# Kernel optimization log

Hardware: AMD Instinct MI355X
Metric: run time of the kernel (lower is better)

The kernel has to match this reference:

```python
import jax, jax.numpy as jnp
import numpy as np

B, T, D, H = 512, 1024, 64, 64     # batch, time, input_size, hidden_size
R = 4                              # number of reward heads
MH = 32                            # MLP hidden size


def setup_inputs() -> dict:
    key = jax.random.key(0)
    ks = jax.random.split(key, 16)
    s = lambda k, shape, scale=1.0: jax.random.normal(k, shape, dtype=jnp.float32) * scale
    inp = {
        "x": s(ks[0], (B, T, D)),
        # learned initial states (nn.Parameter randn(1,1,H) -> store as (H,))
        "h_init": s(ks[1], (H,)),
        "c_init": s(ks[2], (H,)),
        # LSTM params, PyTorch layout: W_ih (4H, D), W_hh (4H, H), gate order i,f,g,o
        "W_ih": s(ks[3], (4 * H, D), 1.0 / np.sqrt(H)),
        "W_hh": s(ks[4], (4 * H, H), 1.0 / np.sqrt(H)),
        "b_ih": s(ks[5], (4 * H,), 1.0 / np.sqrt(H)),
        "b_hh": s(ks[6], (4 * H,), 1.0 / np.sqrt(H)),
        # R stacked MLP heads: Linear(H,MH) -> ReLU -> Linear(MH,MH) -> ReLU -> Linear(MH,1)
        "W1": s(ks[7], (R, MH, H), 1.0 / np.sqrt(H)),
        "b1": s(ks[8], (R, MH), 1.0 / np.sqrt(H)),
        "W2": s(ks[9], (R, MH, MH), 1.0 / np.sqrt(MH)),
        "b2": s(ks[10], (R, MH), 1.0 / np.sqrt(MH)),
        "W3": s(ks[11], (R, 1, MH), 1.0 / np.sqrt(MH)),
        "b3": s(ks[12], (R, 1), 1.0 / np.sqrt(MH)),
    }
    return inp


def _lstm(x, h0, c0, W_ih, W_hh, b_ih, b_hh):
    # x: (B, T, D). Returns y: (B, T, H).
    Hh = h0.shape[-1]
    b = b_ih + b_hh                      # (4H,)
    # precompute input projections for all steps: (T, B, 4H)
    xg = jnp.einsum('btd,gd->tbg', x, W_ih) + b

    def step(carry, xg_t):
        h, c = carry                     # (B, H) each
        gates = xg_t + h @ W_hh.T        # (B, 4H)
        i, f, g, o = jnp.split(gates, 4, axis=-1)
        c = jax.nn.sigmoid(f) * c + jax.nn.sigmoid(i) * jnp.tanh(g)
        h = jax.nn.sigmoid(o) * jnp.tanh(c)
        return (h, c), h

    Bb = x.shape[0]
    h0b = jnp.broadcast_to(h0, (Bb, Hh))
    c0b = jnp.broadcast_to(c0, (Bb, Hh))
    _, ys = jax.lax.scan(step, (h0b, c0b), xg)   # ys: (T, B, H)
    return jnp.transpose(ys, (1, 0, 2))


def _heads(y, W1, b1, W2, b2, W3, b3):
    # y: (B, T, H) -> (R, B, T); all R heads computed in one batched einsum chain
    h1 = jax.nn.relu(jnp.einsum('bth,rmh->rbtm', y, W1) + b1[:, None, None, :])
    h2 = jax.nn.relu(jnp.einsum('rbtm,rnm->rbtn', h1, W2) + b2[:, None, None, :])
    out = jnp.einsum('rbtn,ron->rbto', h2, W3) + b3[:, None, None, :]
    return out[..., 0]                   # squeeze last dim -> (R, B, T)


def reference(x, h_init, c_init, W_ih, W_hh, b_ih, b_hh, W1, b1, W2, b2, W3, b3):
    y = _lstm(x, h_init, c_init, W_ih, W_hh, b_ih, b_hh)
    outs = _heads(y, W1, b1, W2, b2, W3, b3)   # (R, B, T); row r == rewards[r] head
    return (y, outs)
```

## Files before the change

kernel.cpp:

```cpp
#include <hip/hip_runtime.h>

#define BB 512
#define TT 1024
#define DD 64
#define HH 64
#define G4 256
#define RR 4
#define MHH 32
#define BT (BB * TT)
#define Y_SIZE (BB * TT * HH)

typedef _Float16 half8 __attribute__((ext_vector_type(8)));
typedef _Float16 half4 __attribute__((ext_vector_type(4)));
typedef float f32x4 __attribute__((ext_vector_type(4)));

#define MFMA16(a, b, c) __builtin_amdgcn_mfma_f32_16x16x32_f16((a), (b), (c), 0, 0, 0)

__device__ __forceinline__ void wg_barrier_lds() {
    asm volatile("s_waitcnt lgkmcnt(0)" ::: "memory");
    __builtin_amdgcn_s_barrier();
    asm volatile("" ::: "memory");
}

__device__ __forceinline__ float sigm(float x) {
    return __builtin_amdgcn_rcpf(1.0f + __expf(-x));
}
__device__ __forceinline__ float tanh_(float x) {
    return 1.0f - 2.0f * __builtin_amdgcn_rcpf(1.0f + __expf(2.0f * x));
}

__device__ __forceinline__ half8 cvt8(f32x4 a, f32x4 b) {
    half8 h;
    h[0] = (_Float16)a[0]; h[1] = (_Float16)a[1];
    h[2] = (_Float16)a[2]; h[3] = (_Float16)a[3];
    h[4] = (_Float16)b[0]; h[5] = (_Float16)b[1];
    h[6] = (_Float16)b[2]; h[7] = (_Float16)b[3];
    return h;
}

__global__ __launch_bounds__(256) void lstm_kernel(
    const float* __restrict__ x, const float* __restrict__ h_init,
    const float* __restrict__ c_init, const float* __restrict__ W_ih,
    const float* __restrict__ W_hh, const float* __restrict__ b_ih,
    const float* __restrict__ b_hh, float* __restrict__ y)
{
    __shared__ alignas(16) _Float16 xch[2][16][2][DD];
    __shared__ alignas(16) _Float16 hst[2][2][HH];

    const int tid  = threadIdx.x;
    const int wave = tid >> 6;
    const int lane = tid & 63;
    const int col  = lane & 15;
    const int quad = lane >> 4;
    const int sel  = (lane >> 3) & 1;
    const int r_act = lane >> 5;
    const int j    = (wave << 4) + col;
    const bool writer = ((lane >> 4) & 1) == 0;

    const int b0 = blockIdx.x * 2;

    half8 bf[4][4];
    f32x4 biasv[4];
#pragma unroll
    for (int G = 0; G < 4; ++G) {
        const int n = (G << 6) + j;
        const float bs = b_ih[n] + b_hh[n];
        biasv[G][0] = bs; biasv[G][1] = bs; biasv[G][2] = bs; biasv[G][3] = bs;
#pragma unroll
        for (int c = 0; c < 4; ++c) {
            const float* src = (c < 2) ? (W_ih + n * DD + c * 32 + quad * 8)
                                       : (W_hh + n * HH + (c - 2) * 32 + quad * 8);
            f32x4 w0 = *(const f32x4*)src;
            f32x4 w1 = *(const f32x4*)(src + 4);
            bf[G][c] = cvt8(w0, w1);
        }
    }

    float c_state = c_init[j];

    if (tid < 128) {
        const int rr = tid >> 6, jj = tid & 63;
        hst[0][rr][jj] = (_Float16)h_init[jj];
    }
    {
        const int ss = tid >> 4, rr = (tid >> 3) & 1, j0 = (tid & 7) << 3;
        const float* src = x + ((b0 + rr) * TT + ss) * DD + j0;
        f32x4 g0 = *(const f32x4*)src;
        f32x4 g1 = *(const f32x4*)(src + 4);
        *(half8*)&xch[0][ss][rr][j0] = cvt8(g0, g1);
    }
    wg_barrier_lds();

    const int ss_pf = tid >> 4, rr_pf = (tid >> 3) & 1, j0_pf = (tid & 7) << 3;

    f32x4 xacc0, xacc1, xacc2, xacc3;
    {
        const _Float16* xrow = &xch[0][0][sel][0];
        half8 a0 = *(const half8*)(xrow + quad * 8);
        half8 a1 = *(const half8*)(xrow + 32 + quad * 8);
        xacc0 = MFMA16(a0, bf[0][0], biasv[0]); xacc0 = MFMA16(a1, bf[0][1], xacc0);
        xacc1 = MFMA16(a0, bf[1][0], biasv[1]); xacc1 = MFMA16(a1, bf[1][1], xacc1);
        xacc2 = MFMA16(a0, bf[2][0], biasv[2]); xacc2 = MFMA16(a1, bf[2][1], xacc2);
        xacc3 = MFMA16(a0, bf[3][0], biasv[3]); xacc3 = MFMA16(a1, bf[3][1], xacc3);
    }

    for (int ci = 0; ci < 64; ++ci) {
        const int buf = ci & 1;
        const bool pf = (ci + 1) < 64;
        f32x4 g0, g1;
        if (pf) {
            const float* src = x + ((b0 + rr_pf) * TT + ((ci + 1) << 4) + ss_pf) * DD + j0_pf;
            g0 = *(const f32x4*)src;
            g1 = *(const f32x4*)(src + 4);
        }
#pragma unroll
        for (int s = 0; s < 16; ++s) {
            const int t = (ci << 4) + s;
            const int p = s & 1;

            const _Float16* hrow = &hst[p][sel][0];
            half8 a2 = *(const half8*)(hrow + quad * 8);
            half8 a3 = *(const half8*)(hrow + 32 + quad * 8);
            f32x4 acc0 = MFMA16(a2, bf[0][2], xacc0); 
            f32x4 acc1 = MFMA16(a2, bf[1][2], xacc1);
            f32x4 acc2 = MFMA16(a2, bf[2][2], xacc2);
            f32x4 acc3 = MFMA16(a2, bf[3][2], xacc3);
            acc0 = MFMA16(a3, bf[0][3], acc0); acc1 = MFMA16(a3, bf[1][3], acc1);
            acc2 = MFMA16(a3, bf[2][3], acc2); acc3 = MFMA16(a3, bf[3][3], acc3);

            if (t < TT - 1) {
                const _Float16* nx = (s < 15) ? &xch[buf][s + 1][sel][0]
                                              : &xch[buf ^ 1][0][sel][0];
                half8 a0 = *(const half8*)(nx + quad * 8);
                half8 a1 = *(const half8*)(nx + 32 + quad * 8);
                xacc0 = MFMA16(a0, bf[0][0], biasv[0]); xacc0 = MFMA16(a1, bf[0][1], xacc0);
                xacc1 = MFMA16(a0, bf[1][0], biasv[1]); xacc1 = MFMA16(a1, bf[1][1], xacc1);
                xacc2 = MFMA16(a0, bf[2][0], biasv[2]); xacc2 = MFMA16(a1, bf[2][1], xacc2);
                xacc3 = MFMA16(a0, bf[3][0], biasv[3]); xacc3 = MFMA16(a1, bf[3][1], xacc3);
            }

            const float si = sigm(acc0[0]);
            const float sf = sigm(acc1[0]);
            const float tg = tanh_(acc2[0]);
            const float so = sigm(acc3[0]);
            c_state = sf * c_state + si * tg;
            const float hv = so * tanh_(c_state);
            if (writer) {
                hst[p ^ 1][r_act][j] = (_Float16)hv;
                y[((b0 + r_act) * TT + t) * HH + j] = hv;
            }
            if (s == 14 && pf) {
                *(half8*)&xch[buf ^ 1][ss_pf][rr_pf][j0_pf] = cvt8(g0, g1);
            }
            wg_barrier_lds();
        }
    }
}

__global__ __launch_bounds__(256) void heads_kernel(
    const float* __restrict__ y,
    const float* __restrict__ W1, const float* __restrict__ b1,
    const float* __restrict__ W2, const float* __restrict__ b2,
    const float* __restrict__ W3, const float* __restrict__ b3,
    float* __restrict__ outs)
{
    __shared__ alignas(16) _Float16 ybuf[64][72];
    __shared__ alignas(16) _Float16 h1buf[64][136];
    __shared__ alignas(16) _Float16 h2buf[64][136];

    const int tid  = threadIdx.x;
    const int wave = tid >> 6;
    const int lane = tid & 63;
    const int col  = lane & 15;
    const int quad = lane >> 4;
    const int arow = (wave << 4) + col;

    half8 w1f[8][2]; float bias1[8];
#pragma unroll
    for (int nt = 0; nt < 8; ++nt) {
        const int n = nt * 16 + col;
        bias1[nt] = b1[n];
#pragma unroll
        for (int c = 0; c < 2; ++c) {
            const float* src = W1 + n * 64 + c * 32 + quad * 8;
            w1f[nt][c] = cvt8(*(const f32x4*)src, *(const f32x4*)(src + 4));
        }
    }
    half8 w2f[8]; float bias2[8];
#pragma unroll
    for (int nt = 0; nt < 8; ++nt) {
        const int n = nt * 16 + col;
        bias2[nt] = b2[n];
        const float* src = W2 + n * 32 + quad * 8;
        w2f[nt] = cvt8(*(const f32x4*)src, *(const f32x4*)(src + 4));
    }
    const int hd3 = tid >> 6, row3 = tid & 63;
    float w3r[32];
#pragma unroll
    for (int i = 0; i < 32; i += 4) {
        f32x4 v = *(const f32x4*)(W3 + hd3 * 32 + i);
        w3r[i] = v[0]; w3r[i + 1] = v[1]; w3r[i + 2] = v[2]; w3r[i + 3] = v[3];
    }
    const float b3v = b3[hd3];

    for (int st = 0; st < 4; ++st) {
        const long base_row = (long)blockIdx.x * 256 + st * 64;
#pragma unroll
        for (int jj = 0; jj < 4; ++jj) {
            const int off = (jj * 256 + tid) * 4;
            const int row = off >> 6, cc = off & 63;
            f32x4 v = *(const f32x4*)(y + base_row * 64 + off);
            half4 hv = {(_Float16)v[0], (_Float16)v[1], (_Float16)v[2], (_Float16)v[3]};
            *(half4*)&ybuf[row][cc] = hv;
        }
        wg_barrier_lds();

        half8 a0 = *(const half8*)&ybuf[arow][quad * 8];
        half8 a1 = *(const half8*)&ybuf[arow][32 + quad * 8];
#pragma unroll
        for (int nt = 0; nt < 8; ++nt) {
            f32x4 acc = {bias1[nt], bias1[nt], bias1[nt], bias1[nt]};
            acc = MFMA16(a0, w1f[nt][0], acc);
            acc = MFMA16(a1, w1f[nt][1], acc);
#pragma unroll
            for (int r = 0; r < 4; ++r) {
                float v = acc[r] > 0.0f ? acc[r] : 0.0f;
                h1buf[(wave << 4) + (quad << 2) + r][nt * 16 + col] = (_Float16)v;
            }
        }
        wg_barrier_lds();

        half8 ah[4];
#pragma unroll
        for (int hd = 0; hd < 4; ++hd)
            ah[hd] = *(const half8*)&h1buf[arow][hd * 32 + quad * 8];
#pragma unroll
        for (int nt = 0; nt < 8; ++nt) {
            f32x4 acc = {bias2[nt], bias2[nt], bias2[nt], bias2[nt]};
            acc = MFMA16(ah[nt >> 1], w2f[nt], acc);
#pragma unroll
            for (int r = 0; r < 4; ++r) {
                float v = acc[r] > 0.0f ? acc[r] : 0.0f;
                h2buf[(wave << 4) + (quad << 2) + r][nt * 16 + col] = (_Float16)v;
            }
        }
        wg_barrier_lds();

        float acc = b3v;
#pragma unroll
        for (int c = 0; c < 4; ++c) {
            half8 v = *(const half8*)&h2buf[row3][hd3 * 32 + c * 8];
#pragma unroll
            for (int u = 0; u < 8; ++u)
                acc = fmaf((float)v[u], w3r[c * 8 + u], acc);
        }
        outs[(long)hd3 * BT + base_row + row3] = acc;
        wg_barrier_lds();
    }
}

extern "C" void kernel_launch(void* const* d_in, const int* in_sizes, int n_in,
                              void* d_out, int out_size, void* d_ws, size_t ws_size,
                              hipStream_t stream) {
    (void)in_sizes; (void)n_in; (void)out_size; (void)d_ws; (void)ws_size;
    const float* x      = (const float*)d_in[0];
    const float* h_init = (const float*)d_in[1];
    const float* c_init = (const float*)d_in[2];
    const float* W_ih   = (const float*)d_in[3];
    const float* W_hh   = (const float*)d_in[4];
    const float* b_ih   = (const float*)d_in[5];
    const float* b_hh   = (const float*)d_in[6];
    const float* W1     = (const float*)d_in[7];
    const float* b1     = (const float*)d_in[8];
    const float* W2     = (const float*)d_in[9];
    const float* b2     = (const float*)d_in[10];
    const float* W3     = (const float*)d_in[11];
    const float* b3     = (const float*)d_in[12];
    float* y    = (float*)d_out;
    float* outs = y + Y_SIZE;

    lstm_kernel<<<dim3(256), dim3(256), 0, stream>>>(x, h_init, c_init, W_ih, W_hh,
                                                     b_ih, b_hh, y);
    heads_kernel<<<dim3(2048), dim3(256), 0, stream>>>(y, W1, b1, W2, b2, W3, b3, outs);
}
```

Before: 563.7 us.

## Fuse reward MLP heads into LSTM recurrence kernel, pipelined across timesteps

Removes the separate heads kernel and computes the reward MLP heads inside the LSTM time loop. Each wave owns one head. The first layer is computed from the current hidden state, and the second and third layers run one step behind via an LDS buffer, with the reduction done through lane shuffles. This drops the re-read of y from global memory and a second launch. In exchange it adds MFMAs and LDS traffic to the latency-critical serial recurrence, plus a tail epilogue for the last two timesteps.

```diff
diff --git a/kernel.cpp b/kernel.cpp
--- a/kernel.cpp
+++ b/kernel.cpp
@@ -4,9 +4,6 @@
 #define TT 1024
 #define DD 64
 #define HH 64
-#define G4 256
-#define RR 4
-#define MHH 32
 #define BT (BB * TT)
 #define Y_SIZE (BB * TT * HH)
 
@@ -38,14 +35,19 @@
     return h;
 }
 
-__global__ __launch_bounds__(256) void lstm_kernel(
+__global__ __launch_bounds__(256) void lstm_fused_kernel(
     const float* __restrict__ x, const float* __restrict__ h_init,
     const float* __restrict__ c_init, const float* __restrict__ W_ih,
     const float* __restrict__ W_hh, const float* __restrict__ b_ih,
-    const float* __restrict__ b_hh, float* __restrict__ y)
+    const float* __restrict__ b_hh,
+    const float* __restrict__ W1, const float* __restrict__ b1,
+    const float* __restrict__ W2, const float* __restrict__ b2,
+    const float* __restrict__ W3, const float* __restrict__ b3,
+    float* __restrict__ y, float* __restrict__ outs)
 {
     __shared__ alignas(16) _Float16 xch[2][16][2][DD];
     __shared__ alignas(16) _Float16 hst[2][2][HH];
+    __shared__ alignas(16) _Float16 h1w[4][2][2][32];
 
     const int tid  = threadIdx.x;
     const int wave = tid >> 6;
@@ -76,6 +78,31 @@
         }
     }
 
+    half8 w1f[2][2]; f32x4 b1v[2];
+    half8 w2f[2];    f32x4 b2v[2];
+    float w3a, w3b, b3v;
+    {
+        const int hd = wave;
+#pragma unroll
+        for (int nt = 0; nt < 2; ++nt) {
+            const int n = hd * 32 + nt * 16 + col;
+            const float s1 = b1[n];
+            b1v[nt][0] = s1; b1v[nt][1] = s1; b1v[nt][2] = s1; b1v[nt][3] = s1;
+#pragma unroll
+            for (int c = 0; c < 2; ++c) {
+                const float* src = W1 + n * 64 + c * 32 + quad * 8;
+                w1f[nt][c] = cvt8(*(const f32x4*)src, *(const f32x4*)(src + 4));
+            }
+            const float s2 = b2[n];
+            b2v[nt][0] = s2; b2v[nt][1] = s2; b2v[nt][2] = s2; b2v[nt][3] = s2;
+            const float* src2 = W2 + n * 32 + quad * 8;
+            w2f[nt] = cvt8(*(const f32x4*)src2, *(const f32x4*)(src2 + 4));
+        }
+        w3a = W3[hd * 32 + col];
+        w3b = W3[hd * 32 + 16 + col];
+        b3v = b3[hd];
+    }
+
     float c_state = c_init[j];
 
     if (tid < 128) {
@@ -89,6 +116,7 @@
         f32x4 g1 = *(const f32x4*)(src + 4);
         *(half8*)&xch[0][ss][rr][j0] = cvt8(g0, g1);
     }
+    ((unsigned int*)h1w)[tid] = 0u;
     wg_barrier_lds();
 
     const int ss_pf = tid >> 4, rr_pf = (tid >> 3) & 1, j0_pf = (tid & 7) << 3;
@@ -103,6 +131,8 @@
         xacc2 = MFMA16(a0, bf[2][0], biasv[2]); xacc2 = MFMA16(a1, bf[2][1], xacc2);
         xacc3 = MFMA16(a0, bf[3][0], biasv[3]); xacc3 = MFMA16(a1, bf[3][1], xacc3);
     }
+
+    const long outs_base = (long)wave * BT + (b0 + (lane >> 5)) * (long)TT;
 
     for (int ci = 0; ci < 64; ++ci) {
         const int buf = ci & 1;
@@ -121,12 +151,20 @@
             const _Float16* hrow = &hst[p][sel][0];
             half8 a2 = *(const half8*)(hrow + quad * 8);
             half8 a3 = *(const half8*)(hrow + 32 + quad * 8);
-            f32x4 acc0 = MFMA16(a2, bf[0][2], xacc0); 
+            const _Float16* h1p = &h1w[wave][p ^ 1][sel][0];
+            half8 ah = *(const half8*)(h1p + quad * 8);
+
+            f32x4 acc0 = MFMA16(a2, bf[0][2], xacc0);
             f32x4 acc1 = MFMA16(a2, bf[1][2], xacc1);
             f32x4 acc2 = MFMA16(a2, bf[2][2], xacc2);
             f32x4 acc3 = MFMA16(a2, bf[3][2], xacc3);
             acc0 = MFMA16(a3, bf[0][3], acc0); acc1 = MFMA16(a3, bf[1][3], acc1);
             acc2 = MFMA16(a3, bf[2][3], acc2); acc3 = MFMA16(a3, bf[3][3], acc3);
+
+            f32x4 h2a = MFMA16(ah, w2f[0], b2v[0]);
+            f32x4 h2b = MFMA16(ah, w2f[1], b2v[1]);
+            f32x4 p1a = MFMA16(a2, w1f[0][0], b1v[0]); p1a = MFMA16(a3, w1f[0][1], p1a);
+            f32x4 p1b = MFMA16(a2, w1f[1][0], b1v[1]); p1b = MFMA16(a3, w1f[1][1], p1b);
 
             if (t < TT - 1) {
                 const _Float16* nx = (s < 15) ? &xch[buf][s + 1][sel][0]
@@ -139,6 +177,20 @@
                 xacc3 = MFMA16(a0, bf[3][0], biasv[3]); xacc3 = MFMA16(a1, bf[3][1], xacc3);
             }
 
+            {
+                float v0 = fmaxf(h2a[0], 0.0f);
+                float v1 = fmaxf(h2b[0], 0.0f);
+                float part = v0 * w3a + v1 * w3b;
+                part += __shfl_xor(part, 1);
+                part += __shfl_xor(part, 2);
+                part += __shfl_xor(part, 4);
+                part += __shfl_xor(part, 8);
+                if (t >= 2 && (lane & 31) == 0)
+                    outs[outs_base + (t - 2)] = part + b3v;
+            }
+            h1w[wave][p][quad >> 1][((quad & 1) << 4) + col] =
+                (_Float16)fmaxf(((quad & 1) ? p1b : p1a)[0], 0.0f);
+
             const float si = sigm(acc0[0]);
             const float sf = sigm(acc1[0]);
             const float tg = tanh_(acc2[0]);
@@ -155,107 +207,37 @@
             wg_barrier_lds();
         }
     }
-}
-
-__global__ __launch_bounds__(256) void heads_kernel(
-    const float* __restrict__ y,
-    const float* __restrict__ W1, const float* __restrict__ b1,
-    const float* __restrict__ W2, const float* __restrict__ b2,
-    const float* __restrict__ W3, const float* __restrict__ b3,
-    float* __restrict__ outs)
-{
-    __shared__ alignas(16) _Float16 ybuf[64][72];
-    __shared__ alignas(16) _Float16 h1buf[64][136];
-    __shared__ alignas(16) _Float16 h2buf[64][136];
-
-    const int tid  = threadIdx.x;
-    const int wave = tid >> 6;
-    const int lane = tid & 63;
-    const int col  = lane & 15;
-    const int quad = lane >> 4;
-    const int arow = (wave << 4) + col;
-
-    half8 w1f[8][2]; float bias1[8];
-#pragma unroll
-    for (int nt = 0; nt < 8; ++nt) {
-        const int n = nt * 16 + col;
-        bias1[nt] = b1[n];
-#pragma unroll
-        for (int c = 0; c < 2; ++c) {
-            const float* src = W1 + n * 64 + c * 32 + quad * 8;
-            w1f[nt][c] = cvt8(*(const f32x4*)src, *(const f32x4*)(src + 4));
-        }
-    }
-    half8 w2f[8]; float bias2[8];
-#pragma unroll
-    for (int nt = 0; nt < 8; ++nt) {
-        const int n = nt * 16 + col;
-        bias2[nt] = b2[n];
-        const float* src = W2 + n * 32 + quad * 8;
-        w2f[nt] = cvt8(*(const f32x4*)src, *(const f32x4*)(src + 4));
-    }
-    const int hd3 = tid >> 6, row3 = tid & 63;
-    float w3r[32];
-#pragma unroll
-    for (int i = 0; i < 32; i += 4) {
-        f32x4 v = *(const f32x4*)(W3 + hd3 * 32 + i);
-        w3r[i] = v[0]; w3r[i + 1] = v[1]; w3r[i + 2] = v[2]; w3r[i + 3] = v[3];
-    }
-    const float b3v = b3[hd3];
-
-    for (int st = 0; st < 4; ++st) {
-        const long base_row = (long)blockIdx.x * 256 + st * 64;
-#pragma unroll
-        for (int jj = 0; jj < 4; ++jj) {
-            const int off = (jj * 256 + tid) * 4;
-            const int row = off >> 6, cc = off & 63;
-            f32x4 v = *(const f32x4*)(y + base_row * 64 + off);
-            half4 hv = {(_Float16)v[0], (_Float16)v[1], (_Float16)v[2], (_Float16)v[3]};
-            *(half4*)&ybuf[row][cc] = hv;
-        }
-        wg_barrier_lds();
-
-        half8 a0 = *(const half8*)&ybuf[arow][quad * 8];
-        half8 a1 = *(const half8*)&ybuf[arow][32 + quad * 8];
-#pragma unroll
-        for (int nt = 0; nt < 8; ++nt) {
-            f32x4 acc = {bias1[nt], bias1[nt], bias1[nt], bias1[nt]};
-            acc = MFMA16(a0, w1f[nt][0], acc);
-            acc = MFMA16(a1, w1f[nt][1], acc);
-#pragma unroll
-            for (int r = 0; r < 4; ++r) {
-                float v = acc[r] > 0.0f ? acc[r] : 0.0f;
-                h1buf[(wave << 4) + (quad << 2) + r][nt * 16 + col] = (_Float16)v;
-            }
-        }
-        wg_barrier_lds();
-
-        half8 ah[4];
-#pragma unroll
-        for (int hd = 0; hd < 4; ++hd)
-            ah[hd] = *(const half8*)&h1buf[arow][hd * 32 + quad * 8];
-#pragma unroll
-        for (int nt = 0; nt < 8; ++nt) {
-            f32x4 acc = {bias2[nt], bias2[nt], bias2[nt], bias2[nt]};
-            acc = MFMA16(ah[nt >> 1], w2f[nt], acc);
-#pragma unroll
-            for (int r = 0; r < 4; ++r) {
-                float v = acc[r] > 0.0f ? acc[r] : 0.0f;
-                h2buf[(wave << 4) + (quad << 2) + r][nt * 16 + col] = (_Float16)v;
-            }
-        }
-        wg_barrier_lds();
-
-        float acc = b3v;
-#pragma unroll
-        for (int c = 0; c < 4; ++c) {
-            half8 v = *(const half8*)&h2buf[row3][hd3 * 32 + c * 8];
-#pragma unroll
-            for (int u = 0; u < 8; ++u)
-                acc = fmaf((float)v[u], w3r[c * 8 + u], acc);
-        }
-        outs[(long)hd3 * BT + base_row + row3] = acc;
-        wg_barrier_lds();
+
+    {
+        const _Float16* h1p = &h1w[wave][1][sel][0];
+        half8 ah = *(const half8*)(h1p + quad * 8);
+        f32x4 h2a = MFMA16(ah, w2f[0], b2v[0]);
+        f32x4 h2b = MFMA16(ah, w2f[1], b2v[1]);
+        float part = fmaxf(h2a[0], 0.0f) * w3a + fmaxf(h2b[0], 0.0f) * w3b;
+        part += __shfl_xor(part, 1);
+        part += __shfl_xor(part, 2);
+        part += __shfl_xor(part, 4);
+        part += __shfl_xor(part, 8);
+        if ((lane & 31) == 0) outs[outs_base + (TT - 2)] = part + b3v;
+
+        const _Float16* hrow = &hst[0][sel][0];
+        half8 a2 = *(const half8*)(hrow + quad * 8);
+        half8 a3 = *(const half8*)(hrow + 32 + quad * 8);
+        f32x4 p1a = MFMA16(a2, w1f[0][0], b1v[0]); p1a = MFMA16(a3, w1f[0][1], p1a);
+        f32x4 p1b = MFMA16(a2, w1f[1][0], b1v[1]); p1b = MFMA16(a3, w1f[1][1], p1b);
+        h1w[wave][0][quad >> 1][((quad & 1) << 4) + col] =
+            (_Float16)fmaxf(((quad & 1) ? p1b : p1a)[0], 0.0f);
+        asm volatile("s_waitcnt lgkmcnt(0)" ::: "memory");
+        const _Float16* h1q = &h1w[wave][0][sel][0];
+        half8 ah2 = *(const half8*)(h1q + quad * 8);
+        f32x4 q2a = MFMA16(ah2, w2f[0], b2v[0]);
+        f32x4 q2b = MFMA16(ah2, w2f[1], b2v[1]);
+        float part2 = fmaxf(q2a[0], 0.0f) * w3a + fmaxf(q2b[0], 0.0f) * w3b;
+        part2 += __shfl_xor(part2, 1);
+        part2 += __shfl_xor(part2, 2);
+        part2 += __shfl_xor(part2, 4);
+        part2 += __shfl_xor(part2, 8);
+        if ((lane & 31) == 0) outs[outs_base + (TT - 1)] = part2 + b3v;
     }
 }
 
@@ -279,7 +261,7 @@
     float* y    = (float*)d_out;
     float* outs = y + Y_SIZE;
 
-    lstm_kernel<<<dim3(256), dim3(256), 0, stream>>>(x, h_init, c_init, W_ih, W_hh,
-                                                     b_ih, b_hh, y);
-    heads_kernel<<<dim3(2048), dim3(256), 0, stream>>>(y, W1, b1, W2, b2, W3, b3, outs);
-}
+    lstm_fused_kernel<<<dim3(256), dim3(256), 0, stream>>>(
+        x, h_init, c_init, W_ih, W_hh, b_ih, b_hh,
+        W1, b1, W2, b2, W3, b3, y, outs);
+}
```

Measured after the change: 678.4 us. 1.2x slower.
